# Optimization experiments

Hardware: AMD Instinct MI355X
Metric: run time of the kernel (lower is better)

## Reference

```python
import jax, jax.numpy as jnp
import numpy as np

B, T, C, H = 4, 2048, 1024, 16
HD = C // H  # head dim = 64


def setup_inputs() -> dict:
    key = jax.random.key(0)
    k1, k2, k3 = jax.random.split(key, 3)
    scale_in = 1.0 / np.sqrt(C)
    return {
        "x": jax.random.normal(k1, (B, T, C), dtype=jnp.float32),
        "W_attn": jax.random.normal(k2, (C, 3 * C), dtype=jnp.float32) * scale_in,
        "b_attn": jnp.zeros((3 * C,), dtype=jnp.float32),
        "W_proj": jax.random.normal(k3, (C, C), dtype=jnp.float32) * scale_in,
        "b_proj": jnp.zeros((C,), dtype=jnp.float32),
    }


def reference(x, W_attn, b_attn, W_proj, b_proj):
    Bx, Tx, Cx = x.shape
    qkv = x @ W_attn + b_attn                      # [B,T,3C]
    q, k, v = jnp.split(qkv, 3, axis=-1)           # each [B,T,C]
    # [B,T,C] -> [B,H,T,HD]
    q = q.reshape(Bx, Tx, H, HD).transpose(0, 2, 1, 3)
    k = k.reshape(Bx, Tx, H, HD).transpose(0, 2, 1, 3)
    v = v.reshape(Bx, Tx, H, HD).transpose(0, 2, 1, 3)
    att = jnp.einsum("bhqd,bhkd->bhqk", q, k) * (1.0 / np.sqrt(HD))
    causal = jnp.tril(jnp.ones((Tx, Tx), dtype=bool))  # [T,T]
    att = jnp.where(causal[None, None, :, :], att, jnp.float32(-jnp.inf))
    att = jax.nn.softmax(att, axis=-1)
    y = jnp.einsum("bhqk,bhkd->bhqd", att, v)      # [B,H,T,HD]
    y = y.transpose(0, 2, 1, 3).reshape(Bx, Tx, Cx)
    return y @ W_proj + b_proj
```

## Files before the change

### kernel.cpp

```cpp
#include <hip/hip_runtime.h>

typedef _Float16 f16;
typedef __attribute__((ext_vector_type(8))) _Float16 h8;
typedef __attribute__((ext_vector_type(4))) _Float16 h4;
typedef __attribute__((ext_vector_type(8))) short s8;
typedef __attribute__((ext_vector_type(4))) unsigned short u16x4;
typedef __attribute__((ext_vector_type(4))) float f4;
typedef __attribute__((ext_vector_type(16))) float f16x;
typedef __attribute__((ext_vector_type(4))) unsigned u4;

#define MFMA(a, b, c) __builtin_amdgcn_mfma_f32_16x16x32_f16(a, b, c, 0, 0, 0)
#define MFMA32(a, b, c) __builtin_amdgcn_mfma_f32_32x32x16_f16(a, b, c, 0, 0, 0)
#define MFMA32B(a, b, c) __builtin_amdgcn_mfma_f32_32x32x16_bf16(a, b, c, 0, 0, 0)

#define QSCALE 0.18033688011112042f

__device__ __forceinline__ void gload16(const void* g, void* l) {
    __builtin_amdgcn_global_load_lds((const __attribute__((address_space(1))) void*)g,
                                     (__attribute__((address_space(3))) void*)l, 16, 0, 0);
}

__device__ __forceinline__ float fexp2(float x) {
    float r;
    asm("v_exp_f32 %0, %1" : "=v"(r) : "v"(x));
    return r;
}

__device__ __forceinline__ unsigned pkb(float a, float b) {
    unsigned r;
    asm("v_cvt_pk_bf16_f32 %0, %1, %2" : "=v"(r) : "v"(a), "v"(b));
    return r;
}

__device__ __forceinline__ unsigned short bf16rn(float x) {
    unsigned u = __builtin_bit_cast(unsigned, x);
    u += 0x7fffu + ((u >> 16) & 1u);
    return (unsigned short)(u >> 16);
}

__device__ __forceinline__ void plswap(unsigned& a, unsigned& b) {
    asm volatile("v_permlane32_swap_b32 %0, %1" : "+v"(a), "+v"(b));
}


__global__ __launch_bounds__(256) void cvt_f16_kernel(const float* __restrict__ in,
                                                      f16* __restrict__ out, int n8) {
    int i = blockIdx.x * blockDim.x + threadIdx.x;
    if (i >= n8) return;
    const float4* p = (const float4*)in + (size_t)i * 2;
    float4 a = p[0], b = p[1];
    h8 o;
    o[0] = (f16)a.x; o[1] = (f16)a.y; o[2] = (f16)a.z; o[3] = (f16)a.w;
    o[4] = (f16)b.x; o[5] = (f16)b.y; o[6] = (f16)b.z; o[7] = (f16)b.w;
    *((h8*)out + i) = o;
}

__global__ __launch_bounds__(256) void transpose_cvt(const float* __restrict__ in,
                                                     f16* __restrict__ out, int R, int Cc) {
    __shared__ float tile[32][33];
    int tx = threadIdx.x, ty = threadIdx.y;
    int c0 = blockIdx.x * 32, r0 = blockIdx.y * 32;
#pragma unroll
    for (int k = 0; k < 32; k += 8)
        tile[ty + k][tx] = in[(size_t)(r0 + ty + k) * Cc + c0 + tx];
    __syncthreads();
#pragma unroll
    for (int k = 0; k < 32; k += 8)
        out[(size_t)(c0 + ty + k) * R + r0 + tx] = (f16)tile[tx][ty + k];
}


__device__ __forceinline__ void gemm_core(const f16* __restrict__ A, const f16* __restrict__ Bt,
                                          int K, int m0, int n0,
                                          f16* lA, f16* lB, f4 acc[4][4]) {
    const int tid = threadIdx.x, lane = tid & 63, wave = tid >> 6;
    const int wm = (wave >> 1) * 64, wn = (wave & 1) * 64;
    for (int k0 = 0; k0 < K; k0 += 64) {
        __syncthreads();
#pragma unroll
        for (int i = 0; i < 4; i++) {
            int s = i * 256 + wave * 64 + lane;
            int row = s >> 3;
            int gc = ((s & 7) ^ (row & 7)) * 8;
            gload16(A + (size_t)(m0 + row) * K + k0 + gc, lA + (i * 256 + wave * 64) * 8);
        }
#pragma unroll
        for (int i = 0; i < 4; i++) {
            int s = i * 256 + wave * 64 + lane;
            int row = s >> 3;
            int gc = ((s & 7) ^ (row & 7)) * 8;
            gload16(Bt + (size_t)(n0 + row) * K + k0 + gc, lB + (i * 256 + wave * 64) * 8);
        }
        __syncthreads();
#pragma unroll
        for (int kk = 0; kk < 2; kk++) {
            h8 af[4], bg[4];
#pragma unroll
            for (int im = 0; im < 4; im++) {
                int row = wm + im * 16 + (lane & 15);
                int pc = (kk * 4 + (lane >> 4)) ^ (row & 7);
                af[im] = *(const h8*)(lA + row * 64 + pc * 8);
            }
#pragma unroll
            for (int in = 0; in < 4; in++) {
                int row = wn + in * 16 + (lane & 15);
                int pc = (kk * 4 + (lane >> 4)) ^ (row & 7);
                bg[in] = *(const h8*)(lB + row * 64 + pc * 8);
            }
#pragma unroll
            for (int im = 0; im < 4; im++)
#pragma unroll
                for (int in = 0; in < 4; in++)
                    acc[im][in] = MFMA(af[im], bg[in], acc[im][in]);
        }
    }
}


__global__ __launch_bounds__(256) void qkv_gemm(const f16* __restrict__ A, const f16* __restrict__ Bt,
                                                const float* __restrict__ bias,
                                                f16* __restrict__ Qo, f16* __restrict__ Ko,
                                                unsigned short* __restrict__ Vo) {
    __shared__ f16 lA[128 * 64], lB[128 * 64];
    f4 acc[4][4];
    const f4 zz = {0.f, 0.f, 0.f, 0.f};
#pragma unroll
    for (int i = 0; i < 4; i++)
#pragma unroll
        for (int j = 0; j < 4; j++) acc[i][j] = zz;

    const int swz = (blockIdx.x & 7) * 192 + (blockIdx.x >> 3);
    const int nb = swz % 24, mb = swz / 24;
    gemm_core(A, Bt, 1024, mb * 128, nb * 128, lA, lB, acc);

    const int lane = threadIdx.x & 63, wave = threadIdx.x >> 6;
    const int wm = (wave >> 1) * 64, wn = (wave & 1) * 64;
#pragma unroll
    for (int im = 0; im < 4; im++) {
        int m4 = mb * 128 + wm + im * 16 + (lane >> 4) * 4;
        int b = m4 >> 11, t0 = m4 & 2047;
#pragma unroll
        for (int in = 0; in < 4; in++) {
            int n = nb * 128 + wn + in * 16 + (lane & 15);
            float bb = bias[n];
            int sec = n >> 10, cc = n & 1023, hh = cc >> 6, d = cc & 63;
            if (sec == 2) {
                u16x4 pv;
#pragma unroll
                for (int r = 0; r < 4; r++) pv[r] = bf16rn(acc[im][in][r] + bb);
                *(u16x4*)(Vo + ((size_t)(b * 16 + hh) * 64 + d) * 2048 + t0) = pv;
            } else {
                f16* dst = sec ? Ko : Qo;
                float sc = sec ? 1.0f : QSCALE;
                size_t base = ((size_t)(b * 16 + hh) * 2048 + t0) * 64 + d;
#pragma unroll
                for (int r = 0; r < 4; r++)
                    dst[base + (size_t)r * 64] = (f16)((acc[im][in][r] + bb) * sc);
            }
        }
    }
}


__global__ __launch_bounds__(256) void proj_gemm(const f16* __restrict__ A, const f16* __restrict__ Bt,
                                                 const float* __restrict__ bias,
                                                 float* __restrict__ out) {
    __shared__ f16 lA[128 * 64], lB[128 * 64];
    f4 acc[4][4];
    const f4 zz = {0.f, 0.f, 0.f, 0.f};
#pragma unroll
    for (int i = 0; i < 4; i++)
#pragma unroll
        for (int j = 0; j < 4; j++) acc[i][j] = zz;

    const int swz = (blockIdx.x & 7) * 64 + (blockIdx.x >> 3);
    const int nb = swz & 7, mb = swz >> 3;
    gemm_core(A, Bt, 1024, mb * 128, nb * 128, lA, lB, acc);

    const int lane = threadIdx.x & 63, wave = threadIdx.x >> 6;
    const int wm = (wave >> 1) * 64, wn = (wave & 1) * 64;
#pragma unroll
    for (int im = 0; im < 4; im++) {
        int m4 = mb * 128 + wm + im * 16 + (lane >> 4) * 4;
#pragma unroll
        for (int in = 0; in < 4; in++) {
            int n = nb * 128 + wn + in * 16 + (lane & 15);
            float bb = bias[n];
#pragma unroll
            for (int r = 0; r < 4; r++)
                out[(size_t)(m4 + r) * 1024 + n] = acc[im][in][r] + bb;
        }
    }
}


#define ASM_VMCNT(N) asm volatile("s_waitcnt vmcnt(" #N ")" ::: "memory")

__device__ __forceinline__ void attn_tile(int k0, bool last, bool stage_next,
                                          int lane, int hi, int ln,
                                          const f16* __restrict__ Kb,
                                          const unsigned short* __restrict__ Vb,
                                          const f16* lKcur, f16* lKnxt,
                                          const h8 (&qf)[4], s8 (&vf)[2][2], s8 (&vfn)[2][2],
                                          float& lpart, f16x& y0, f16x& y1) {
    if (stage_next) {
#pragma unroll
        for (int i = 0; i < 4; i++) {
            int s = i * 64 + lane;
            int row = s >> 3;
            int gc = ((s & 7) ^ (row & 7)) * 8;
            gload16(Kb + (size_t)(k0 + 32 + row) * 64 + gc, lKnxt + i * 512);
        }
#pragma unroll
        for (int ks = 0; ks < 2; ks++)
#pragma unroll
            for (int j = 0; j < 2; j++)
                vfn[ks][j] = *(const s8*)(Vb + (size_t)(j * 32 + ln) * 2048 + (k0 + 32) +
                                          ks * 16 + hi * 8);
        ASM_VMCNT(8);
    } else {
        ASM_VMCNT(0);
    }
    __builtin_amdgcn_sched_barrier(0);

    f16x s0;
#pragma unroll
    for (int r = 0; r < 16; r++) s0[r] = 0.f;
    __builtin_amdgcn_s_setprio(1);
#pragma unroll
    for (int dd = 0; dd < 4; dd++) {
        const int c = (dd * 2 + hi) ^ (ln & 7);
        h8 ka = *(const h8*)(lKcur + ln * 64 + c * 8);
        s0 = MFMA32(ka, qf[dd], s0);
    }
    __builtin_amdgcn_s_setprio(0);

    if (last) {
#pragma unroll
        for (int r = 0; r < 16; r++) {
            int kl = (r & 3) + 8 * (r >> 2) + 4 * hi;
            if (kl > ln) s0[r] = -3e38f;
        }
    }

    float ls = 0.f;
#pragma unroll
    for (int r = 0; r < 16; r++) {
        float p = fexp2(s0[r]);
        s0[r] = p;
        ls += p;
    }
    lpart += ls;

    s8 pa[2];
    {
        unsigned a0 = pkb(s0[0], s0[1]), a1 = pkb(s0[2], s0[3]);
        unsigned b0 = pkb(s0[4], s0[5]), b1 = pkb(s0[6], s0[7]);
        plswap(a0, b0); plswap(a1, b1);
        u4 w0; w0[0] = a0; w0[1] = a1; w0[2] = b0; w0[3] = b1;
        pa[0] = __builtin_bit_cast(s8, w0);
        unsigned c0 = pkb(s0[8], s0[9]), c1 = pkb(s0[10], s0[11]);
        unsigned d0 = pkb(s0[12], s0[13]), d1 = pkb(s0[14], s0[15]);
        plswap(c0, d0); plswap(c1, d1);
        u4 w1; w1[0] = c0; w1[1] = c1; w1[2] = d0; w1[3] = d1;
        pa[1] = __builtin_bit_cast(s8, w1);
    }

    __builtin_amdgcn_s_setprio(1);
#pragma unroll
    for (int ks = 0; ks < 2; ks++) {
        y0 = MFMA32B(pa[ks], vf[ks][0], y0);
        y1 = MFMA32B(pa[ks], vf[ks][1], y1);
    }
    __builtin_amdgcn_s_setprio(0);
}

__global__ __launch_bounds__(64) void attn_kernel(const f16* __restrict__ Q,
                                                  const f16* __restrict__ K,
                                                  const unsigned short* __restrict__ Vg,
                                                  f16* __restrict__ O) {
    __shared__ f16 lK[2][2048];
    const int lane = threadIdx.x;
    const int hi = lane >> 5, ln = lane & 31;
    const int bh = blockIdx.x & 63;
    const int p = (int)(blockIdx.x >> 6);
    const f16* Qb = Q + (size_t)bh * 2048 * 64;
    const f16* Kb = K + (size_t)bh * 2048 * 64;
    const unsigned short* Vb = Vg + (size_t)bh * 64 * 2048;
    const int b = bh >> 4, hh = bh & 15;

    for (int ph = 0; ph < 2; ph++) {
        const int qt = ph ? p : 63 - p;
        const int qw = qt * 32;

        h8 qf[4];
#pragma unroll
        for (int dd = 0; dd < 4; dd++)
            qf[dd] = *(const h8*)(Qb + (size_t)(qw + ln) * 64 + dd * 16 + hi * 8);

        float lpart = 0.f;
        f16x y0, y1;
#pragma unroll
        for (int r = 0; r < 16; r++) { y0[r] = 0.f; y1[r] = 0.f; }

        const int nt = qt + 1;

        s8 vfA[2][2], vfB[2][2];
#pragma unroll
        for (int i = 0; i < 4; i++) {
            int s = i * 64 + lane;
            int row = s >> 3;
            int gc = ((s & 7) ^ (row & 7)) * 8;
            gload16(Kb + (size_t)row * 64 + gc, &lK[0][i * 512]);
        }
#pragma unroll
        for (int ks = 0; ks < 2; ks++)
#pragma unroll
            for (int j = 0; j < 2; j++)
                vfA[ks][j] = *(const s8*)(Vb + (size_t)(j * 32 + ln) * 2048 + ks * 16 + hi * 8);

        for (int it = 0; it < nt; it += 2) {
            attn_tile(it * 32, it == nt - 1, it + 1 < nt, lane, hi, ln, Kb, Vb,
                      &lK[0][0], &lK[1][0], qf, vfA, vfB, lpart, y0, y1);
            if (it + 1 < nt)
                attn_tile((it + 1) * 32, it + 1 == nt - 1, it + 2 < nt, lane, hi, ln, Kb, Vb,
                          &lK[1][0], &lK[0][0], qf, vfB, vfA, lpart, y0, y1);
        }

        float lT = lpart + __shfl_xor(lpart, 32);
        float inv = 1.0f / lT;
#pragma unroll
        for (int r = 0; r < 16; r++) {
            int crow = (r & 3) + 8 * (r >> 2) + 4 * hi;
            float invr = __shfl(inv, crow);
            size_t base = ((size_t)(b * 2048 + qw + crow)) * 1024 + hh * 64 + ln;
            O[base] = (f16)(y0[r] * invr);
            O[base + 32] = (f16)(y1[r] * invr);
        }
    }
}


extern "C" void kernel_launch(void* const* d_in, const int* in_sizes, int n_in,
                              void* d_out, int out_size, void* d_ws, size_t ws_size,
                              hipStream_t stream) {
    const float* x      = (const float*)d_in[0];
    const float* W_attn = (const float*)d_in[1];
    const float* b_attn = (const float*)d_in[2];
    const float* W_proj = (const float*)d_in[3];
    const float* b_proj = (const float*)d_in[4];
    float* out = (float*)d_out;

    char* ws = (char*)d_ws;
    f16* xb  = (f16*)ws;
    f16* Wat = (f16*)(ws + 16777216);
    f16* Wpt = (f16*)(ws + 16777216 + 6291456);
    unsigned short* Vt = (unsigned short*)(ws + 16777216 + 6291456 + 2097152);
    f16* Qs  = (f16*)d_out;
    f16* Ks  = (f16*)((char*)d_out + 16777216);

    cvt_f16_kernel<<<4096, 256, 0, stream>>>(x, xb, 1048576);
    transpose_cvt<<<dim3(96, 32), dim3(32, 8), 0, stream>>>(W_attn, Wat, 1024, 3072);
    transpose_cvt<<<dim3(32, 32), dim3(32, 8), 0, stream>>>(W_proj, Wpt, 1024, 1024);
    qkv_gemm<<<1536, 256, 0, stream>>>(xb, Wat, b_attn, Qs, Ks, Vt);
    attn_kernel<<<2048, 64, 0, stream>>>(Qs, Ks, Vt, xb);
    proj_gemm<<<512, 256, 0, stream>>>(xb, Wpt, b_proj, out);
}
```

Baseline: 206.0 us.

## Load K fragments directly to registers and tile V by 32-key blocks

The attention kernel stops staging K through shared memory with global_load_lds and instead loads each lane's K fragments straight into registers, double-buffered like V. The QKV GEMM writes V in a blocked layout of 32 keys by 64 dims so each tile's V reads fall in one contiguous 4KB chunk. The row-sum of exponentials becomes a tree reduction. The aim is to drop the LDS round-trip and give V loads better locality, at the cost of more VGPRs and uncoalesced per-lane K loads.

```diff
diff --git a/kernel.cpp b/kernel.cpp
--- a/kernel.cpp
+++ b/kernel.cpp
@@ -148,7 +148,8 @@
                 u16x4 pv;
 #pragma unroll
                 for (int r = 0; r < 4; r++) pv[r] = bf16rn(acc[im][in][r] + bb);
-                *(u16x4*)(Vo + ((size_t)(b * 16 + hh) * 64 + d) * 2048 + t0) = pv;
+                *(u16x4*)(Vo + (size_t)(b * 16 + hh) * 131072 + (t0 >> 5) * 2048 + d * 32 +
+                          (t0 & 31)) = pv;
             } else {
                 f16* dst = sec ? Ko : Qo;
                 float sc = sec ? 1.0f : QSCALE;
@@ -200,22 +201,20 @@
                                           int lane, int hi, int ln,
                                           const f16* __restrict__ Kb,
                                           const unsigned short* __restrict__ Vb,
-                                          const f16* lKcur, f16* lKnxt,
-                                          const h8 (&qf)[4], s8 (&vf)[2][2], s8 (&vfn)[2][2],
+                                          const h8 (&qf)[4],
+                                          h8 (&kf)[4], h8 (&kfn)[4],
+                                          s8 (&vf)[2][2], s8 (&vfn)[2][2],
                                           float& lpart, f16x& y0, f16x& y1) {
     if (stage_next) {
-#pragma unroll
-        for (int i = 0; i < 4; i++) {
-            int s = i * 64 + lane;
-            int row = s >> 3;
-            int gc = ((s & 7) ^ (row & 7)) * 8;
-            gload16(Kb + (size_t)(k0 + 32 + row) * 64 + gc, lKnxt + i * 512);
-        }
+        const int kn = k0 + 32;
+#pragma unroll
+        for (int dd = 0; dd < 4; dd++)
+            kfn[dd] = *(const h8*)(Kb + (size_t)(kn + ln) * 64 + dd * 16 + hi * 8);
 #pragma unroll
         for (int ks = 0; ks < 2; ks++)
 #pragma unroll
             for (int j = 0; j < 2; j++)
-                vfn[ks][j] = *(const s8*)(Vb + (size_t)(j * 32 + ln) * 2048 + (k0 + 32) +
+                vfn[ks][j] = *(const s8*)(Vb + (size_t)(kn >> 5) * 2048 + (j * 32 + ln) * 32 +
                                           ks * 16 + hi * 8);
         ASM_VMCNT(8);
     } else {
@@ -228,11 +227,7 @@
     for (int r = 0; r < 16; r++) s0[r] = 0.f;
     __builtin_amdgcn_s_setprio(1);
 #pragma unroll
-    for (int dd = 0; dd < 4; dd++) {
-        const int c = (dd * 2 + hi) ^ (ln & 7);
-        h8 ka = *(const h8*)(lKcur + ln * 64 + c * 8);
-        s0 = MFMA32(ka, qf[dd], s0);
-    }
+    for (int dd = 0; dd < 4; dd++) s0 = MFMA32(kf[dd], qf[dd], s0);
     __builtin_amdgcn_s_setprio(0);
 
     if (last) {
@@ -243,14 +238,17 @@
         }
     }
 
-    float ls = 0.f;
+    float ps[16];
 #pragma unroll
     for (int r = 0; r < 16; r++) {
-        float p = fexp2(s0[r]);
-        s0[r] = p;
-        ls += p;
-    }
-    lpart += ls;
+        ps[r] = fexp2(s0[r]);
+        s0[r] = ps[r];
+    }
+#pragma unroll
+    for (int m = 1; m < 16; m <<= 1)
+#pragma unroll
+        for (int r = 0; r < 16; r += 2 * m) ps[r] += ps[r + m];
+    lpart += ps[0];
 
     s8 pa[2];
     {
@@ -279,14 +277,13 @@
                                                   const f16* __restrict__ K,
                                                   const unsigned short* __restrict__ Vg,
                                                   f16* __restrict__ O) {
-    __shared__ f16 lK[2][2048];
     const int lane = threadIdx.x;
     const int hi = lane >> 5, ln = lane & 31;
     const int bh = blockIdx.x & 63;
     const int p = (int)(blockIdx.x >> 6);
     const f16* Qb = Q + (size_t)bh * 2048 * 64;
     const f16* Kb = K + (size_t)bh * 2048 * 64;
-    const unsigned short* Vb = Vg + (size_t)bh * 64 * 2048;
+    const unsigned short* Vb = Vg + (size_t)bh * 131072;
     const int b = bh >> 4, hh = bh & 15;
 
     for (int ph = 0; ph < 2; ph++) {
@@ -305,26 +302,23 @@
 
         const int nt = qt + 1;
 
+        h8 kfA[4], kfB[4];
         s8 vfA[2][2], vfB[2][2];
 #pragma unroll
-        for (int i = 0; i < 4; i++) {
-            int s = i * 64 + lane;
-            int row = s >> 3;
-            int gc = ((s & 7) ^ (row & 7)) * 8;
-            gload16(Kb + (size_t)row * 64 + gc, &lK[0][i * 512]);
-        }
+        for (int dd = 0; dd < 4; dd++)
+            kfA[dd] = *(const h8*)(Kb + (size_t)ln * 64 + dd * 16 + hi * 8);
 #pragma unroll
         for (int ks = 0; ks < 2; ks++)
 #pragma unroll
             for (int j = 0; j < 2; j++)
-                vfA[ks][j] = *(const s8*)(Vb + (size_t)(j * 32 + ln) * 2048 + ks * 16 + hi * 8);
+                vfA[ks][j] = *(const s8*)(Vb + (size_t)(j * 32 + ln) * 32 + ks * 16 + hi * 8);
 
         for (int it = 0; it < nt; it += 2) {
             attn_tile(it * 32, it == nt - 1, it + 1 < nt, lane, hi, ln, Kb, Vb,
-                      &lK[0][0], &lK[1][0], qf, vfA, vfB, lpart, y0, y1);
+                      qf, kfA, kfB, vfA, vfB, lpart, y0, y1);
             if (it + 1 < nt)
                 attn_tile((it + 1) * 32, it + 1 == nt - 1, it + 2 < nt, lane, hi, ln, Kb, Vb,
-                          &lK[1][0], &lK[0][0], qf, vfB, vfA, lpart, y0, y1);
+                          qf, kfB, kfA, vfB, vfA, lpart, y0, y1);
         }
 
         float lT = lpart + __shfl_xor(lpart, 32);
```

Measured after the change: 216.5 us. 5.1% more time.

## Process both paired query tiles in one KV sweep and tile V layout

Applied to the files above, without the earlier changes.

The attention kernel used to run two sequential passes over K/V, one per paired query tile (63-p and p). It now does a single pass over the key tiles, loads each K tile from LDS into registers once, and applies it to both query tiles while the shorter tile is still in range, so K/V traffic for the shared prefix is halved. V is now written by the QKV GEMM in 32-token blocked layout, which makes the per-tile V loads contiguous. The row-sum reduction becomes a tree. In exchange, the second set of accumulators and Q fragments raises register pressure, which may cost occupancy or cause spills.

```diff
diff --git a/kernel.cpp b/kernel.cpp
--- a/kernel.cpp
+++ b/kernel.cpp
@@ -148,7 +148,8 @@
                 u16x4 pv;
 #pragma unroll
                 for (int r = 0; r < 4; r++) pv[r] = bf16rn(acc[im][in][r] + bb);
-                *(u16x4*)(Vo + ((size_t)(b * 16 + hh) * 64 + d) * 2048 + t0) = pv;
+                *(u16x4*)(Vo + (size_t)(b * 16 + hh) * 131072 + (t0 >> 5) * 2048 + d * 32 +
+                          (t0 & 31)) = pv;
             } else {
                 f16* dst = sec ? Ko : Qo;
                 float sc = sec ? 1.0f : QSCALE;
@@ -196,26 +197,65 @@
 
 #define ASM_VMCNT(N) asm volatile("s_waitcnt vmcnt(" #N ")" ::: "memory")
 
-__device__ __forceinline__ void attn_tile(int k0, bool last, bool stage_next,
+__device__ __forceinline__ void sm_pv(f16x& s, float& lpart, f16x& y0, f16x& y1,
+                                      const s8 (&vf)[2][2]) {
+    float ps[16];
+#pragma unroll
+    for (int r = 0; r < 16; r++) {
+        ps[r] = fexp2(s[r]);
+        s[r] = ps[r];
+    }
+#pragma unroll
+    for (int m = 1; m < 16; m <<= 1)
+#pragma unroll
+        for (int r = 0; r < 16; r += 2 * m) ps[r] += ps[r + m];
+    lpart += ps[0];
+
+    s8 pa[2];
+    {
+        unsigned a0 = pkb(s[0], s[1]), a1 = pkb(s[2], s[3]);
+        unsigned b0 = pkb(s[4], s[5]), b1 = pkb(s[6], s[7]);
+        plswap(a0, b0); plswap(a1, b1);
+        u4 w0; w0[0] = a0; w0[1] = a1; w0[2] = b0; w0[3] = b1;
+        pa[0] = __builtin_bit_cast(s8, w0);
+        unsigned c0 = pkb(s[8], s[9]), c1 = pkb(s[10], s[11]);
+        unsigned d0 = pkb(s[12], s[13]), d1 = pkb(s[14], s[15]);
+        plswap(c0, d0); plswap(c1, d1);
+        u4 w1; w1[0] = c0; w1[1] = c1; w1[2] = d0; w1[3] = d1;
+        pa[1] = __builtin_bit_cast(s8, w1);
+    }
+
+    __builtin_amdgcn_s_setprio(1);
+#pragma unroll
+    for (int ks = 0; ks < 2; ks++) {
+        y0 = MFMA32B(pa[ks], vf[ks][0], y0);
+        y1 = MFMA32B(pa[ks], vf[ks][1], y1);
+    }
+    __builtin_amdgcn_s_setprio(0);
+}
+
+__device__ __forceinline__ void attn_tile(int kt, int qtA, int qtB, int nt,
                                           int lane, int hi, int ln,
                                           const f16* __restrict__ Kb,
                                           const unsigned short* __restrict__ Vb,
                                           const f16* lKcur, f16* lKnxt,
-                                          const h8 (&qf)[4], s8 (&vf)[2][2], s8 (&vfn)[2][2],
-                                          float& lpart, f16x& y0, f16x& y1) {
-    if (stage_next) {
+                                          const h8 (&qfA)[4], const h8 (&qfB)[4],
+                                          s8 (&vf)[2][2], s8 (&vfn)[2][2],
+                                          float& lpA, float& lpB,
+                                          f16x& yA0, f16x& yA1, f16x& yB0, f16x& yB1) {
+    if (kt + 1 < nt) {
 #pragma unroll
         for (int i = 0; i < 4; i++) {
             int s = i * 64 + lane;
             int row = s >> 3;
             int gc = ((s & 7) ^ (row & 7)) * 8;
-            gload16(Kb + (size_t)(k0 + 32 + row) * 64 + gc, lKnxt + i * 512);
+            gload16(Kb + (size_t)((kt + 1) * 32 + row) * 64 + gc, lKnxt + i * 512);
         }
 #pragma unroll
         for (int ks = 0; ks < 2; ks++)
 #pragma unroll
             for (int j = 0; j < 2; j++)
-                vfn[ks][j] = *(const s8*)(Vb + (size_t)(j * 32 + ln) * 2048 + (k0 + 32) +
+                vfn[ks][j] = *(const s8*)(Vb + (size_t)(kt + 1) * 2048 + (j * 32 + ln) * 32 +
                                           ks * 16 + hi * 8);
         ASM_VMCNT(8);
     } else {
@@ -223,56 +263,49 @@
     }
     __builtin_amdgcn_sched_barrier(0);
 
-    f16x s0;
-#pragma unroll
-    for (int r = 0; r < 16; r++) s0[r] = 0.f;
-    __builtin_amdgcn_s_setprio(1);
+    h8 kr[4];
 #pragma unroll
     for (int dd = 0; dd < 4; dd++) {
         const int c = (dd * 2 + hi) ^ (ln & 7);
-        h8 ka = *(const h8*)(lKcur + ln * 64 + c * 8);
-        s0 = MFMA32(ka, qf[dd], s0);
-    }
+        kr[dd] = *(const h8*)(lKcur + ln * 64 + c * 8);
+    }
+
+    f16x sA;
+#pragma unroll
+    for (int r = 0; r < 16; r++) sA[r] = 0.f;
+    __builtin_amdgcn_s_setprio(1);
+#pragma unroll
+    for (int dd = 0; dd < 4; dd++) sA = MFMA32(kr[dd], qfA[dd], sA);
     __builtin_amdgcn_s_setprio(0);
 
-    if (last) {
+    if (kt == qtA) {
 #pragma unroll
         for (int r = 0; r < 16; r++) {
             int kl = (r & 3) + 8 * (r >> 2) + 4 * hi;
-            if (kl > ln) s0[r] = -3e38f;
-        }
-    }
-
-    float ls = 0.f;
-#pragma unroll
-    for (int r = 0; r < 16; r++) {
-        float p = fexp2(s0[r]);
-        s0[r] = p;
-        ls += p;
-    }
-    lpart += ls;
-
-    s8 pa[2];
-    {
-        unsigned a0 = pkb(s0[0], s0[1]), a1 = pkb(s0[2], s0[3]);
-        unsigned b0 = pkb(s0[4], s0[5]), b1 = pkb(s0[6], s0[7]);
-        plswap(a0, b0); plswap(a1, b1);
-        u4 w0; w0[0] = a0; w0[1] = a1; w0[2] = b0; w0[3] = b1;
-        pa[0] = __builtin_bit_cast(s8, w0);
-        unsigned c0 = pkb(s0[8], s0[9]), c1 = pkb(s0[10], s0[11]);
-        unsigned d0 = pkb(s0[12], s0[13]), d1 = pkb(s0[14], s0[15]);
-        plswap(c0, d0); plswap(c1, d1);
-        u4 w1; w1[0] = c0; w1[1] = c1; w1[2] = d0; w1[3] = d1;
-        pa[1] = __builtin_bit_cast(s8, w1);
-    }
-
-    __builtin_amdgcn_s_setprio(1);
-#pragma unroll
-    for (int ks = 0; ks < 2; ks++) {
-        y0 = MFMA32B(pa[ks], vf[ks][0], y0);
-        y1 = MFMA32B(pa[ks], vf[ks][1], y1);
-    }
-    __builtin_amdgcn_s_setprio(0);
+            if (kl > ln) sA[r] = -3e38f;
+        }
+    }
+
+    if (kt <= qtB) {
+        f16x sB;
+#pragma unroll
+        for (int r = 0; r < 16; r++) sB[r] = 0.f;
+        __builtin_amdgcn_s_setprio(1);
+#pragma unroll
+        for (int dd = 0; dd < 4; dd++) sB = MFMA32(kr[dd], qfB[dd], sB);
+        __builtin_amdgcn_s_setprio(0);
+        if (kt == qtB) {
+#pragma unroll
+            for (int r = 0; r < 16; r++) {
+                int kl = (r & 3) + 8 * (r >> 2) + 4 * hi;
+                if (kl > ln) sB[r] = -3e38f;
+            }
+        }
+        sm_pv(sA, lpA, yA0, yA1, vf);
+        sm_pv(sB, lpB, yB0, yB1, vf);
+    } else {
+        sm_pv(sA, lpA, yA0, yA1, vf);
+    }
 }
 
 __global__ __launch_bounds__(64) void attn_kernel(const f16* __restrict__ Q,
@@ -284,58 +317,71 @@
     const int hi = lane >> 5, ln = lane & 31;
     const int bh = blockIdx.x & 63;
     const int p = (int)(blockIdx.x >> 6);
+    const int qtA = 63 - p, qtB = p;
+    const int qwA = qtA * 32, qwB = qtB * 32;
     const f16* Qb = Q + (size_t)bh * 2048 * 64;
     const f16* Kb = K + (size_t)bh * 2048 * 64;
-    const unsigned short* Vb = Vg + (size_t)bh * 64 * 2048;
+    const unsigned short* Vb = Vg + (size_t)bh * 131072;
     const int b = bh >> 4, hh = bh & 15;
 
-    for (int ph = 0; ph < 2; ph++) {
-        const int qt = ph ? p : 63 - p;
-        const int qw = qt * 32;
-
-        h8 qf[4];
-#pragma unroll
-        for (int dd = 0; dd < 4; dd++)
-            qf[dd] = *(const h8*)(Qb + (size_t)(qw + ln) * 64 + dd * 16 + hi * 8);
-
-        float lpart = 0.f;
-        f16x y0, y1;
-#pragma unroll
-        for (int r = 0; r < 16; r++) { y0[r] = 0.f; y1[r] = 0.f; }
-
-        const int nt = qt + 1;
-
-        s8 vfA[2][2], vfB[2][2];
-#pragma unroll
-        for (int i = 0; i < 4; i++) {
-            int s = i * 64 + lane;
-            int row = s >> 3;
-            int gc = ((s & 7) ^ (row & 7)) * 8;
-            gload16(Kb + (size_t)row * 64 + gc, &lK[0][i * 512]);
-        }
-#pragma unroll
-        for (int ks = 0; ks < 2; ks++)
-#pragma unroll
-            for (int j = 0; j < 2; j++)
-                vfA[ks][j] = *(const s8*)(Vb + (size_t)(j * 32 + ln) * 2048 + ks * 16 + hi * 8);
-
-        for (int it = 0; it < nt; it += 2) {
-            attn_tile(it * 32, it == nt - 1, it + 1 < nt, lane, hi, ln, Kb, Vb,
-                      &lK[0][0], &lK[1][0], qf, vfA, vfB, lpart, y0, y1);
-            if (it + 1 < nt)
-                attn_tile((it + 1) * 32, it + 1 == nt - 1, it + 2 < nt, lane, hi, ln, Kb, Vb,
-                          &lK[1][0], &lK[0][0], qf, vfB, vfA, lpart, y0, y1);
-        }
-
-        float lT = lpart + __shfl_xor(lpart, 32);
+    h8 qfA[4], qfB[4];
+#pragma unroll
+    for (int dd = 0; dd < 4; dd++) {
+        qfA[dd] = *(const h8*)(Qb + (size_t)(qwA + ln) * 64 + dd * 16 + hi * 8);
+        qfB[dd] = *(const h8*)(Qb + (size_t)(qwB + ln) * 64 + dd * 16 + hi * 8);
+    }
+
+    float lpA = 0.f, lpB = 0.f;
+    f16x yA0, yA1, yB0, yB1;
+#pragma unroll
+    for (int r = 0; r < 16; r++) { yA0[r] = 0.f; yA1[r] = 0.f; yB0[r] = 0.f; yB1[r] = 0.f; }
+
+    const int nt = qtA + 1;
+
+    s8 vfA[2][2], vfB[2][2];
+#pragma unroll
+    for (int i = 0; i < 4; i++) {
+        int s = i * 64 + lane;
+        int row = s >> 3;
+        int gc = ((s & 7) ^ (row & 7)) * 8;
+        gload16(Kb + (size_t)row * 64 + gc, &lK[0][i * 512]);
+    }
+#pragma unroll
+    for (int ks = 0; ks < 2; ks++)
+#pragma unroll
+        for (int j = 0; j < 2; j++)
+            vfA[ks][j] = *(const s8*)(Vb + (size_t)(j * 32 + ln) * 32 + ks * 16 + hi * 8);
+
+    for (int kt = 0; kt < nt; kt += 2) {
+        attn_tile(kt, qtA, qtB, nt, lane, hi, ln, Kb, Vb, &lK[0][0], &lK[1][0],
+                  qfA, qfB, vfA, vfB, lpA, lpB, yA0, yA1, yB0, yB1);
+        if (kt + 1 < nt)
+            attn_tile(kt + 1, qtA, qtB, nt, lane, hi, ln, Kb, Vb, &lK[1][0], &lK[0][0],
+                      qfA, qfB, vfB, vfA, lpA, lpB, yA0, yA1, yB0, yB1);
+    }
+
+    {
+        float lT = lpA + __shfl_xor(lpA, 32);
         float inv = 1.0f / lT;
 #pragma unroll
         for (int r = 0; r < 16; r++) {
             int crow = (r & 3) + 8 * (r >> 2) + 4 * hi;
             float invr = __shfl(inv, crow);
-            size_t base = ((size_t)(b * 2048 + qw + crow)) * 1024 + hh * 64 + ln;
-            O[base] = (f16)(y0[r] * invr);
-            O[base + 32] = (f16)(y1[r] * invr);
+            size_t base = ((size_t)(b * 2048 + qwA + crow)) * 1024 + hh * 64 + ln;
+            O[base] = (f16)(yA0[r] * invr);
+            O[base + 32] = (f16)(yA1[r] * invr);
+        }
+    }
+    {
+        float lT = lpB + __shfl_xor(lpB, 32);
+        float inv = 1.0f / lT;
+#pragma unroll
+        for (int r = 0; r < 16; r++) {
+            int crow = (r & 3) + 8 * (r >> 2) + 4 * hi;
+            float invr = __shfl(inv, crow);
+            size_t base = ((size_t)(b * 2048 + qwB + crow)) * 1024 + hh * 64 + ln;
+            O[base] = (f16)(yB0[r] * invr);
+            O[base + 32] = (f16)(yB1[r] * invr);
         }
     }
 }
```

Result: faster. 201.5 us (-2.2%).
